# Kernel tuning notes

Hardware: AMD Instinct MI355X
Metric: run time of the kernel (lower is better)

The kernel has to match this reference:

```python
import jax, jax.numpy as jnp
import numpy as np
import math

PATCHES = [(2, 2), (4, 4), (8, 8), (16, 16)]  # (width, height) per scale
D_MODEL = 256
EPS = 1e-5


def setup_inputs() -> dict:
    key = jax.random.key(0)
    ks = jax.random.split(key, 12)
    b, c, h, w = 4, D_MODEL, 128, 128
    s = 1.0 / math.sqrt(c)
    inp = {
        'x': jax.random.normal(ks[0], (b, c, h, w), jnp.float32),
        'y': jax.random.normal(ks[1], (b, c, h, w), jnp.float32),
        'Wq': jax.random.normal(ks[2], (c, c), jnp.float32) * s,
        'bq': jnp.zeros((c,), jnp.float32),
        'Wk': jax.random.normal(ks[3], (c, c), jnp.float32) * s,
        'bk': jnp.zeros((c,), jnp.float32),
        'Wv': jax.random.normal(ks[4], (c, c), jnp.float32) * s,
        'bv': jnp.zeros((c,), jnp.float32),
        'Wo': jax.random.normal(ks[5], (c, c, 3, 3), jnp.float32) * (1.0 / math.sqrt(c * 9)),
        'bo': jnp.zeros((c,), jnp.float32),
        'gamma': jnp.ones((c,), jnp.float32),
        'beta': jnp.zeros((c,), jnp.float32),
    }
    return inp


def _conv1x1(x, W, b):
    # 1x1 conv == channel matmul
    return jnp.einsum('oc,bchw->bohw', W, x) + b[None, :, None, None]


def _windowed_attention(q, k, v, ww, hh):
    # q,k,v: [b, d_k, h, w] -> windows of (hh, ww), tokens = out_h*out_w
    b, d_k, h, w = q.shape
    out_h, out_w = h // hh, w // ww

    def to_tokens(t):
        t = t.reshape(b, d_k, out_h, hh, out_w, ww)
        t = t.transpose(0, 2, 4, 1, 3, 5)  # b, out_h, out_w, d_k, hh, ww
        return t.reshape(b, out_h * out_w, d_k * hh * ww)

    qt, kt, vt = to_tokens(q), to_tokens(k), to_tokens(v)
    scale = 1.0 / math.sqrt(qt.shape[-1])
    scores = jnp.einsum('bnd,bmd->bnm', qt, kt) * scale
    p = jax.nn.softmax(scores, axis=-1)
    out = jnp.einsum('bnm,bmd->bnd', p, vt)
    out = out.reshape(b, out_h, out_w, d_k, hh, ww)
    out = out.transpose(0, 3, 1, 4, 2, 5).reshape(b, d_k, h, w)
    return out


def reference(x, y, Wq, bq, Wk, bk, Wv, bv, Wo, bo, gamma, beta):
    b, c, h, w = x.shape
    n_scales = len(PATCHES)
    d_k = c // n_scales

    q_all = _conv1x1(x, Wq, bq)
    k_all = _conv1x1(y, Wk, bk)
    v_all = _conv1x1(y, Wv, bv)

    outs = []
    for i, (ww, hh) in enumerate(PATCHES):
        sl = slice(i * d_k, (i + 1) * d_k)
        outs.append(_windowed_attention(q_all[:, sl], k_all[:, sl], v_all[:, sl], ww, hh))
    out = jnp.concatenate(outs, axis=1)  # [b, c, h, w]

    # output_linear: Conv3x3 (pad 1) -> BatchNorm2d (batch stats) -> LeakyReLU(0.2)
    z = jax.lax.conv_general_dilated(
        out, Wo, window_strides=(1, 1), padding='SAME',
        dimension_numbers=('NCHW', 'OIHW', 'NCHW')) + bo[None, :, None, None]
    mean = jnp.mean(z, axis=(0, 2, 3), keepdims=True)
    var = jnp.var(z, axis=(0, 2, 3), keepdims=True)
    zn = (z - mean) * jax.lax.rsqrt(var + EPS)
    zn = zn * gamma[None, :, None, None] + beta[None, :, None, None]
    return jnp.where(zn >= 0, zn, 0.2 * zn)
```

## Files before the change

### kernel.cpp

```cpp
#include <hip/hip_runtime.h>
#include <math.h>

#define BN 4
#define CC 256
#define HH_ 128
#define WW_ 128
#define HWP (HH_*WW_)
#define TOK (64*HWP)


typedef __attribute__((ext_vector_type(8))) short bf16x8;
typedef __attribute__((ext_vector_type(4))) float f32x4;

__device__ __forceinline__ float bf2f(unsigned short u) {
    return __uint_as_float(((unsigned)u) << 16);
}
__device__ __forceinline__ unsigned short f2bf(float f) {
    unsigned u = __float_as_uint(f);
    u += 0x7FFF + ((u >> 16) & 1);
    return (unsigned short)(u >> 16);
}
__device__ __forceinline__ void load4f(const unsigned short* p, float o[4]) {
    ushort4 v = *(const ushort4*)p;
    o[0] = bf2f(v.x); o[1] = bf2f(v.y); o[2] = bf2f(v.z); o[3] = bf2f(v.w);
}
__device__ __forceinline__ float ld1(const unsigned short* p) { return bf2f(*p); }
__device__ __forceinline__ float ld1(const float* p) { return *p; }
__device__ __forceinline__ void st1(unsigned short* p, float v) { *p = f2bf(v); }
__device__ __forceinline__ void st1(float* p, float v) { *p = v; }

#define LDS_STRIDE 72

struct Tile32 { uint4 v[4]; };

__device__ __forceinline__ Tile32 load_tile_bf16(
    const unsigned short* src, size_t stride, int t)
{
    int r = t >> 1, kc = (t & 1) * 32;
    const uint4* sp = (const uint4*)(src + (size_t)r * stride + kc);
    Tile32 o;
    o.v[0] = sp[0]; o.v[1] = sp[1]; o.v[2] = sp[2]; o.v[3] = sp[3];
    return o;
}

__device__ __forceinline__ Tile32 load_tile_f32(
    const float* src, size_t stride, int t)
{
    int r = t >> 1, kc = (t & 1) * 32;
    const float4* sp = (const float4*)(src + (size_t)r * stride + kc);
    unsigned short tmp[32];
    #pragma unroll
    for (int i = 0; i < 8; i++) {
        float4 v = sp[i];
        tmp[i*4+0] = f2bf(v.x); tmp[i*4+1] = f2bf(v.y);
        tmp[i*4+2] = f2bf(v.z); tmp[i*4+3] = f2bf(v.w);
    }
    Tile32 o;
    const uint4* tp = (const uint4*)tmp;
    o.v[0] = tp[0]; o.v[1] = tp[1]; o.v[2] = tp[2]; o.v[3] = tp[3];
    return o;
}

__device__ __forceinline__ void store_tile(
    unsigned short* lds, const Tile32& d, int t)
{
    int r = t >> 1, kc = (t & 1) * 32;
    uint4* dp = (uint4*)&lds[r * LDS_STRIDE + kc];
    dp[0] = d.v[0]; dp[1] = d.v[1]; dp[2] = d.v[2]; dp[3] = d.v[3];
}

__device__ __forceinline__ void mfma_iter(
    const unsigned short* As, const unsigned short* Bs,
    int wm, int wn, int lr, int quad, f32x4 acc[4][4])
{
    #pragma unroll
    for (int s = 0; s < 2; s++) {
        bf16x8 af[4], bfr[4];
        #pragma unroll
        for (int i = 0; i < 4; i++)
            af[i] = *(const bf16x8*)&As[(wm*64 + i*16 + lr) * LDS_STRIDE + s*32 + quad*8];
        #pragma unroll
        for (int j = 0; j < 4; j++)
            bfr[j] = *(const bf16x8*)&Bs[(wn*64 + j*16 + lr) * LDS_STRIDE + s*32 + quad*8];
        #pragma unroll
        for (int i = 0; i < 4; i++)
            #pragma unroll
            for (int j = 0; j < 4; j++)
                acc[i][j] = __builtin_amdgcn_mfma_f32_16x16x32_bf16(
                    af[i], bfr[j], acc[i][j], 0, 0, 0);
    }
}

__global__ __launch_bounds__(256) void zero_kernel(float* __restrict__ p)
{
    p[blockIdx.x * 256 + threadIdx.x] = 0.f;
}

__global__ __launch_bounds__(256) void nchw_to_nhwc(
    const float* __restrict__ x, const float* __restrict__ y,
    unsigned short* __restrict__ xt, unsigned short* __restrict__ yt)
{
    __shared__ unsigned short T[64 * 72];
    int z = blockIdx.z;
    int b = z & 3, which = z >> 2;
    const float* src = (which ? y : x) + (size_t)b * CC * HWP;
    unsigned short* dst = (which ? yt : xt) + (size_t)b * HWP * CC;
    int p0 = blockIdx.x * 64, c0 = blockIdx.y * 64;
    int t = threadIdx.x;

    int cl = t >> 2, pc = (t & 3) * 16;
    #pragma unroll
    for (int e = 0; e < 16; e += 4) {
        float4 v = *(const float4*)&src[(size_t)(c0 + cl) * HWP + p0 + pc + e];
        T[(pc + e + 0) * 72 + cl] = f2bf(v.x);
        T[(pc + e + 1) * 72 + cl] = f2bf(v.y);
        T[(pc + e + 2) * 72 + cl] = f2bf(v.z);
        T[(pc + e + 3) * 72 + cl] = f2bf(v.w);
    }
    __syncthreads();
    int p = t >> 2, cc = (t & 3) * 16;
    uint4 a = *(uint4*)&T[p * 72 + cc];
    uint4 bsec = *(uint4*)&T[p * 72 + cc + 8];
    uint4* dp = (uint4*)&dst[(size_t)(p0 + p) * CC + c0 + cc];
    dp[0] = a; dp[1] = bsec;
}

__global__ __launch_bounds__(256) void wpack_kernel(
    const float* __restrict__ Wo, unsigned short* __restrict__ wpack)
{
    int o = blockIdx.x, c = threadIdx.x;
    const float* wr = Wo + ((size_t)o * CC + c) * 9;
    #pragma unroll
    for (int tap = 0; tap < 9; tap++)
        wpack[((size_t)o * 9 + tap) * CC + c] = f2bf(wr[tap]);
}

__global__ __launch_bounds__(256) void proj_gemm(
    const unsigned short* __restrict__ xt, const unsigned short* __restrict__ yt,
    const float* __restrict__ Wq, const float* __restrict__ bq,
    const float* __restrict__ Wk, const float* __restrict__ bk,
    const float* __restrict__ Wv, const float* __restrict__ bv,
    unsigned short* __restrict__ qt, unsigned short* __restrict__ kt,
    unsigned short* __restrict__ vt)
{
    __shared__ unsigned short As[128 * LDS_STRIDE], Bs[128 * LDS_STRIDE];
    int z = blockIdx.z, b = z & 3, which = z >> 2;
    const unsigned short* src = (which == 0) ? xt : yt;
    const float* Wm   = (which == 0) ? Wq : (which == 1 ? Wk : Wv);
    const float* bias = (which == 0) ? bq : (which == 1 ? bk : bv);
    unsigned short* outp = (which == 0) ? qt : (which == 1 ? kt : vt);

    int m0 = blockIdx.y * 128;
    int n0 = blockIdx.x * 128;
    const float* A = Wm + (size_t)m0 * CC;
    const unsigned short* B = src + ((size_t)b * HWP + n0) * CC;

    int t = threadIdx.x, w = t >> 6, lane = t & 63;
    int quad = lane >> 4, lr = lane & 15, wm = w >> 1, wn = w & 1;

    f32x4 acc[4][4];
    #pragma unroll
    for (int i = 0; i < 4; i++)
        #pragma unroll
        for (int j = 0; j < 4; j++) acc[i][j] = (f32x4){0.f, 0.f, 0.f, 0.f};

    for (int k0 = 0; k0 < CC; k0 += 64) {
        Tile32 ta = load_tile_f32(A + k0, CC, t);
        Tile32 tb = load_tile_bf16(B + k0, CC, t);
        __syncthreads();
        store_tile(As, ta, t); store_tile(Bs, tb, t);
        __syncthreads();
        mfma_iter(As, Bs, wm, wn, lr, quad, acc);
    }

    #pragma unroll
    for (int i = 0; i < 4; i++) {
        int obase = m0 + wm * 64 + i * 16 + quad * 4;
        #pragma unroll
        for (int rr = 0; rr < 4; rr++) {
            int o = obase + rr;
            int s = o >> 6, lg = s + 1;
            int ch = o & 63;
            float bia = bias[o];
            unsigned short* ob = outp + ((size_t)s * 4 + b) * TOK;
            #pragma unroll
            for (int j = 0; j < 4; j++) {
                int p = n0 + wn * 64 + j * 16 + lr;
                int yy = p >> 7, xx = p & 127;
                int oy = yy >> lg, wy = yy & ((1 << lg) - 1);
                int ox = xx >> lg, wx = xx & ((1 << lg) - 1);
                int tokn = (oy << (7 - lg)) + ox;
                int didx = (ch << (2 * lg)) + (wy << lg) + wx;
                size_t idx;
                if (which == 2 && s < 3)
                    idx = ((size_t)didx << (14 - 2 * lg)) + tokn;
                else
                    idx = ((size_t)tokn << (6 + 2 * lg)) + didx;
                ob[idx] = f2bf(acc[i][j][rr] + bia);
            }
        }
    }
}

template<int NTOK, int DD>
__global__ __launch_bounds__(256) void s_gemm_exp(
    const unsigned short* __restrict__ Qb, const unsigned short* __restrict__ Kb,
    unsigned short* __restrict__ S0, unsigned short* __restrict__ S1,
    float* __restrict__ rsg, float sc)
{
    __shared__ unsigned short As[128 * LDS_STRIDE], Bs[128 * LDS_STRIDE];
    int bz = blockIdx.z;
    int m0 = blockIdx.y * 128, n0 = blockIdx.x * 128;
    const unsigned short* Q = Qb + (size_t)bz * TOK + (size_t)m0 * DD;
    const unsigned short* K = Kb + (size_t)bz * TOK + (size_t)n0 * DD;
    unsigned short* S;
    if (S1) S = bz ? S1 : S0;
    else    S = S0 + (size_t)bz * NTOK * NTOK;
    float* rs = rsg + (size_t)bz * NTOK;

    int t = threadIdx.x, w = t >> 6, lane = t & 63;
    int quad = lane >> 4, lr = lane & 15, wm = w >> 1, wn = w & 1;

    f32x4 acc[4][4];
    #pragma unroll
    for (int i = 0; i < 4; i++)
        #pragma unroll
        for (int j = 0; j < 4; j++) acc[i][j] = (f32x4){0.f, 0.f, 0.f, 0.f};

    for (int k0 = 0; k0 < DD; k0 += 64) {
        Tile32 ta = load_tile_bf16(Q + k0, DD, t);
        Tile32 tb = load_tile_bf16(K + k0, DD, t);
        __syncthreads();
        store_tile(As, ta, t); store_tile(Bs, tb, t);
        __syncthreads();
        mfma_iter(As, Bs, wm, wn, lr, quad, acc);
    }

    #pragma unroll
    for (int i = 0; i < 4; i++) {
        int m = m0 + wm * 64 + i * 16 + quad * 4;
        float rsum[4] = {0.f, 0.f, 0.f, 0.f};
        #pragma unroll
        for (int j = 0; j < 4; j++) {
            int n = n0 + wn * 64 + j * 16 + lr;
            #pragma unroll
            for (int rr = 0; rr < 4; rr++) {
                float e = __expf(acc[i][j][rr] * sc);
                S[(size_t)(m + rr) * NTOK + n] = f2bf(e);
                rsum[rr] += e;
            }
        }
        #pragma unroll
        for (int rr = 0; rr < 4; rr++) {
            float v = rsum[rr];
            v += __shfl_xor(v, 1);
            v += __shfl_xor(v, 2);
            v += __shfl_xor(v, 4);
            v += __shfl_xor(v, 8);
            if (lr == 0) atomicAdd(&rs[m + rr], v);
        }
    }
}

template<int NTOK, int DD, int LG, int CH0>
__global__ __launch_bounds__(256) void o_gemm(
    const unsigned short* __restrict__ Pb, const unsigned short* __restrict__ Vb,
    const float* __restrict__ rsg, unsigned short* __restrict__ aot, int b0)
{
    __shared__ unsigned short As[128 * LDS_STRIDE], Bs[128 * LDS_STRIDE];
    int bz = blockIdx.z, b = b0 + bz;
    int m0 = blockIdx.y * 128, n0 = blockIdx.x * 128;
    const unsigned short* P = Pb + (size_t)bz * NTOK * NTOK + (size_t)m0 * NTOK;
    const unsigned short* V = Vb + (size_t)bz * TOK + (size_t)n0 * NTOK;
    const float* rs = rsg + (size_t)bz * NTOK;

    int t = threadIdx.x, w = t >> 6, lane = t & 63;
    int quad = lane >> 4, lr = lane & 15, wm = w >> 1, wn = w & 1;

    f32x4 acc[4][4];
    #pragma unroll
    for (int i = 0; i < 4; i++)
        #pragma unroll
        for (int j = 0; j < 4; j++) acc[i][j] = (f32x4){0.f, 0.f, 0.f, 0.f};

    for (int k0 = 0; k0 < NTOK; k0 += 64) {
        Tile32 ta = load_tile_bf16(P + k0, NTOK, t);
        Tile32 tb = load_tile_bf16(V + k0, NTOK, t);
        __syncthreads();
        store_tile(As, ta, t); store_tile(Bs, tb, t);
        __syncthreads();
        mfma_iter(As, Bs, wm, wn, lr, quad, acc);
    }

    #pragma unroll
    for (int i = 0; i < 4; i++) {
        int tb0 = m0 + wm * 64 + i * 16 + quad * 4;
        #pragma unroll
        for (int rr = 0; rr < 4; rr++) {
            int tokn = tb0 + rr;
            float inv = 1.f / rs[tokn];
            int oy = tokn >> (7 - LG), ox = tokn & ((1 << (7 - LG)) - 1);
            #pragma unroll
            for (int j = 0; j < 4; j++) {
                int d = n0 + wn * 64 + j * 16 + lr;
                int ch = d >> (2 * LG);
                int r2 = d & ((1 << (2 * LG)) - 1);
                int wy = r2 >> LG, wx = r2 & ((1 << LG) - 1);
                int yy = (oy << LG) + wy, xx = (ox << LG) + wx;
                aot[((size_t)b * HWP + yy * WW_ + xx) * CC + CH0 + ch] =
                    f2bf(acc[i][j][rr] * inv);
            }
        }
    }
}

__global__ __launch_bounds__(256) void o0_split(
    const unsigned short* __restrict__ P0, const unsigned short* __restrict__ P1,
    const unsigned short* __restrict__ Vb, float* __restrict__ part)
{
    __shared__ unsigned short As[128 * LDS_STRIDE], Bs[128 * LDS_STRIDE];
    int bz = blockIdx.z;
    int bsel = bz >> 2, sp = bz & 3;
    int m0 = blockIdx.y * 128;
    int n0 = blockIdx.x * 128;
    const unsigned short* P = (bsel ? P1 : P0) + (size_t)m0 * 4096 + sp * 1024;
    const unsigned short* V = Vb + (size_t)bsel * TOK + (size_t)n0 * 4096 + sp * 1024;
    float* op = part + (size_t)bz * TOK;

    int t = threadIdx.x, w = t >> 6, lane = t & 63;
    int quad = lane >> 4, lr = lane & 15, wm = w >> 1, wn = w & 1;

    f32x4 acc[4][4];
    #pragma unroll
    for (int i = 0; i < 4; i++)
        #pragma unroll
        for (int j = 0; j < 4; j++) acc[i][j] = (f32x4){0.f, 0.f, 0.f, 0.f};

    for (int k0 = 0; k0 < 1024; k0 += 64) {
        Tile32 ta = load_tile_bf16(P + k0, 4096, t);
        Tile32 tb = load_tile_bf16(V + k0, 4096, t);
        __syncthreads();
        store_tile(As, ta, t); store_tile(Bs, tb, t);
        __syncthreads();
        mfma_iter(As, Bs, wm, wn, lr, quad, acc);
    }

    #pragma unroll
    for (int i = 0; i < 4; i++) {
        int tb0 = m0 + wm * 64 + i * 16 + quad * 4;
        #pragma unroll
        for (int rr = 0; rr < 4; rr++) {
            int tokn = tb0 + rr;
            #pragma unroll
            for (int j = 0; j < 4; j++) {
                int d = n0 + wn * 64 + j * 16 + lr;
                op[(size_t)tokn * 256 + d] = acc[i][j][rr];
            }
        }
    }
}

__global__ __launch_bounds__(256) void combine0(
    const float* __restrict__ part, const float* __restrict__ rs,
    unsigned short* __restrict__ aot, int b0)
{
    int bsel = blockIdx.y, b = b0 + bsel;
    int tok0 = blockIdx.x * 16;
    const float* p = part + (size_t)bsel * 4 * TOK;
    int t = threadIdx.x;
    int w = t >> 6, ch = t & 63;
    int wy = w >> 1, wx = w & 1;
    #pragma unroll 4
    for (int u = 0; u < 16; u++) {
        int tok = tok0 + u;
        size_t base = (size_t)tok * 256 + ch * 4 + w;
        float v = p[base] + p[base + TOK] + p[base + 2 * (size_t)TOK]
                + p[base + 3 * (size_t)TOK];
        v *= 1.f / rs[(size_t)bsel * 4096 + tok];
        int oy = tok >> 6, ox = tok & 63;
        int yy = oy * 2 + wy, xx = ox * 2 + wx;
        aot[((size_t)b * HWP + yy * WW_ + xx) * CC + ch] = f2bf(v);
    }
}

__device__ __forceinline__ Tile32 load_tile_conv(
    const unsigned short* aob, int ys, int dx, int cbase, int t)
{
    int r = t >> 1, kc = (t & 1) * 32;
    int xs = r + dx;
    Tile32 o;
    if (ys >= 0 && ys < HH_ && xs >= 0 && xs < WW_) {
        const uint4* sp = (const uint4*)(aob + ((size_t)ys * WW_ + xs) * CC + cbase + kc);
        o.v[0] = sp[0]; o.v[1] = sp[1]; o.v[2] = sp[2]; o.v[3] = sp[3];
    } else {
        uint4 zz = make_uint4(0, 0, 0, 0);
        o.v[0] = zz; o.v[1] = zz; o.v[2] = zz; o.v[3] = zz;
    }
    return o;
}

__global__ __launch_bounds__(256) void conv_gemm(
    const unsigned short* __restrict__ aot, const unsigned short* __restrict__ wpack,
    const float* __restrict__ bo, float* __restrict__ zout)
{
    __shared__ unsigned short As[128 * LDS_STRIDE], Bs[128 * LDS_STRIDE];
    int yrow = blockIdx.x;
    int o0 = blockIdx.y * 128;
    int b = blockIdx.z;
    const unsigned short* aob = aot + (size_t)b * HWP * CC;
    const unsigned short* wsrc = wpack + (size_t)o0 * 2304;

    int t = threadIdx.x, w = t >> 6, lane = t & 63;
    int quad = lane >> 4, lr = lane & 15, wm = w >> 1, wn = w & 1;

    f32x4 acc[4][4];
    #pragma unroll
    for (int i = 0; i < 4; i++)
        #pragma unroll
        for (int j = 0; j < 4; j++) acc[i][j] = (f32x4){0.f, 0.f, 0.f, 0.f};

    for (int tap = 0; tap < 9; tap++) {
        int dy = tap / 3 - 1, dx = tap % 3 - 1;
        int ys = yrow + dy;
        for (int cb = 0; cb < CC; cb += 64) {
            Tile32 ta = load_tile_bf16(wsrc + tap * CC + cb, 2304, t);
            Tile32 tb = load_tile_conv(aob, ys, dx, cb, t);
            __syncthreads();
            store_tile(As, ta, t); store_tile(Bs, tb, t);
            __syncthreads();
            mfma_iter(As, Bs, wm, wn, lr, quad, acc);
        }
    }

    #pragma unroll
    for (int i = 0; i < 4; i++) {
        int ob = o0 + wm * 64 + i * 16 + quad * 4;
        #pragma unroll
        for (int j = 0; j < 4; j++) {
            int x = wn * 64 + j * 16 + lr;
            #pragma unroll
            for (int rr = 0; rr < 4; rr++) {
                int o = ob + rr;
                zout[((size_t)(b * CC + o)) * HWP + yrow * WW_ + x] =
                    acc[i][j][rr] + bo[o];
            }
        }
    }
}

__global__ __launch_bounds__(256) void s3_kernel(
    const unsigned short* __restrict__ Qb, const unsigned short* __restrict__ Kb,
    float* __restrict__ S, float sc)
{
    const int N = 64, D = 16384, KLEN = 1024;
    int b = blockIdx.z >> 4, kc = blockIdx.z & 15;
    const unsigned short* Q = Qb + (size_t)b * TOK;
    const unsigned short* K = Kb + (size_t)b * TOK;
    float* Sb = S + (size_t)b * N * N;
    int k0 = kc * KLEN;

    __shared__ float As[16][64], Bs[16][64];
    int t = threadIdx.x, tx = t & 15, ty = t >> 4, r = t >> 2, q = t & 3;

    float acc[4][4] = {};
    for (int kk = k0; kk < k0 + KLEN; kk += 16) {
        float a4[4], b4[4];
        load4f(&Q[(size_t)r * D + kk + q * 4], a4);
        load4f(&K[(size_t)r * D + kk + q * 4], b4);
        __syncthreads();
        As[q*4+0][r] = a4[0]; As[q*4+1][r] = a4[1]; As[q*4+2][r] = a4[2]; As[q*4+3][r] = a4[3];
        Bs[q*4+0][r] = b4[0]; Bs[q*4+1][r] = b4[1]; Bs[q*4+2][r] = b4[2]; Bs[q*4+3][r] = b4[3];
        __syncthreads();
        #pragma unroll
        for (int k = 0; k < 16; k++) {
            float4 af = *(const float4*)&As[k][ty*4];
            float4 bf = *(const float4*)&Bs[k][tx*4];
            float ar[4] = {af.x, af.y, af.z, af.w};
            float br[4] = {bf.x, bf.y, bf.z, bf.w};
            #pragma unroll
            for (int ii = 0; ii < 4; ii++)
                #pragma unroll
                for (int jj = 0; jj < 4; jj++)
                    acc[ii][jj] = fmaf(ar[ii], br[jj], acc[ii][jj]);
        }
    }

    #pragma unroll
    for (int ii = 0; ii < 4; ii++)
        #pragma unroll
        for (int jj = 0; jj < 4; jj++)
            atomicAdd(&Sb[(size_t)(ty * 4 + ii) * N + tx * 4 + jj], acc[ii][jj] * sc);
}

template<typename T>
__global__ __launch_bounds__(256) void softmax_kernel(T* __restrict__ S, int n)
{
    int b = blockIdx.y;
    int row = blockIdx.x;
    T* rp = S + (size_t)b * n * n + (size_t)row * n;
    __shared__ float red[256];
    int t = threadIdx.x;

    float m = -1e30f;
    for (int j = t; j < n; j += 256) m = fmaxf(m, ld1(&rp[j]));
    red[t] = m; __syncthreads();
    for (int s = 128; s > 0; s >>= 1) { if (t < s) red[t] = fmaxf(red[t], red[t + s]); __syncthreads(); }
    m = red[0]; __syncthreads();

    float sum = 0.f;
    for (int j = t; j < n; j += 256) { float e = __expf(ld1(&rp[j]) - m); st1(&rp[j], e); sum += e; }
    red[t] = sum; __syncthreads();
    for (int s = 128; s > 0; s >>= 1) { if (t < s) red[t] += red[t + s]; __syncthreads(); }
    float inv = 1.f / red[0];
    for (int j = t; j < n; j += 256) st1(&rp[j], ld1(&rp[j]) * inv);
}

__global__ __launch_bounds__(256) void o3_kernel(
    const float* __restrict__ P, const unsigned short* __restrict__ Vb,
    unsigned short* __restrict__ aot)
{
    const int N = 64, D = 16384, LG = 4, CH0 = 192;
    int bz = blockIdx.z;
    const float* Pb = P + (size_t)bz * N * N;
    const unsigned short* V = Vb + (size_t)bz * TOK;
    int i0 = blockIdx.x * 64, d0 = blockIdx.y * 64;

    __shared__ float Ps[16][64];
    __shared__ float Vs[16][64];
    int t = threadIdx.x, tx = t & 15, ty = t >> 4, r = t >> 2, q = t & 3;
    int vr = t >> 4, vq = t & 15;

    float acc[4][4] = {};
    for (int j0 = 0; j0 < N; j0 += 16) {
        float p4[4], v4[4];
        float4 pv = *(const float4*)&Pb[(size_t)(i0 + r) * N + j0 + q * 4];
        p4[0] = pv.x; p4[1] = pv.y; p4[2] = pv.z; p4[3] = pv.w;
        load4f(&V[(size_t)(j0 + vr) * D + d0 + vq * 4], v4);
        __syncthreads();
        Ps[q*4+0][r] = p4[0]; Ps[q*4+1][r] = p4[1]; Ps[q*4+2][r] = p4[2]; Ps[q*4+3][r] = p4[3];
        Vs[vr][vq*4+0] = v4[0]; Vs[vr][vq*4+1] = v4[1]; Vs[vr][vq*4+2] = v4[2]; Vs[vr][vq*4+3] = v4[3];
        __syncthreads();
        #pragma unroll
        for (int k = 0; k < 16; k++) {
            float4 pf = *(const float4*)&Ps[k][ty*4];
            float4 vf = *(const float4*)&Vs[k][tx*4];
            float pr[4] = {pf.x, pf.y, pf.z, pf.w};
            float vrr[4] = {vf.x, vf.y, vf.z, vf.w};
            #pragma unroll
            for (int ii = 0; ii < 4; ii++)
                #pragma unroll
                for (int jj = 0; jj < 4; jj++)
                    acc[ii][jj] = fmaf(pr[ii], vrr[jj], acc[ii][jj]);
        }
    }

    #pragma unroll
    for (int ii = 0; ii < 4; ii++) {
        int tokn = i0 + ty * 4 + ii;
        int oy = tokn >> (7 - LG), ox = tokn & ((1 << (7 - LG)) - 1);
        #pragma unroll
        for (int jj = 0; jj < 4; jj++) {
            int d = d0 + tx * 4 + jj;
            int ch = d >> (2 * LG);
            int r2 = d & ((1 << (2 * LG)) - 1);
            int wy = r2 >> LG, wx = r2 & ((1 << LG) - 1);
            int yy = (oy << LG) + wy, xx = (ox << LG) + wx;
            aot[((size_t)bz * HWP + yy * WW_ + xx) * CC + CH0 + ch] = f2bf(acc[ii][jj]);
        }
    }
}

__global__ __launch_bounds__(256) void bn_stats_kernel(
    const float* __restrict__ z, const float* __restrict__ gamma,
    const float* __restrict__ beta, float* __restrict__ stats)
{
    int c = blockIdx.x;
    int t = threadIdx.x;
    float s = 0.f, s2 = 0.f;
    for (int i = t; i < BN * HWP; i += 256) {
        int b = i >> 14, p = i & (HWP - 1);
        float v = z[(((size_t)b * CC + c) << 14) + p];
        s += v; s2 = fmaf(v, v, s2);
    }
    __shared__ float r1[256], r2[256];
    r1[t] = s; r2[t] = s2; __syncthreads();
    for (int st = 128; st > 0; st >>= 1) {
        if (t < st) { r1[t] += r1[t + st]; r2[t] += r2[t + st]; }
        __syncthreads();
    }
    if (t == 0) {
        float inv_n = 1.f / (BN * HWP);
        float mean = r1[0] * inv_n;
        float var = r2[0] * inv_n - mean * mean;
        float rstd = rsqrtf(var + 1e-5f);
        float gs = gamma[c] * rstd;
        stats[c] = gs;
        stats[CC + c] = beta[c] - mean * gs;
    }
}

__global__ __launch_bounds__(256) void bn_apply_kernel(
    float* __restrict__ z, const float* __restrict__ stats)
{
    size_t i4 = (size_t)blockIdx.x * 256 + threadIdx.x;
    size_t idx = i4 * 4;
    int c = (int)((idx >> 14) & 255);
    float gs = stats[c], gb = stats[CC + c];
    float4 v = *(float4*)&z[idx];
    v.x = fmaf(v.x, gs, gb); v.y = fmaf(v.y, gs, gb);
    v.z = fmaf(v.z, gs, gb); v.w = fmaf(v.w, gs, gb);
    v.x = v.x >= 0.f ? v.x : 0.2f * v.x;
    v.y = v.y >= 0.f ? v.y : 0.2f * v.y;
    v.z = v.z >= 0.f ? v.z : 0.2f * v.z;
    v.w = v.w >= 0.f ? v.w : 0.2f * v.w;
    *(float4*)&z[idx] = v;
}

extern "C" void kernel_launch(void* const* d_in, const int* in_sizes, int n_in,
                              void* d_out, int out_size, void* d_ws, size_t ws_size,
                              hipStream_t stream)
{
    const float* x     = (const float*)d_in[0];
    const float* y     = (const float*)d_in[1];
    const float* Wq    = (const float*)d_in[2];
    const float* bq    = (const float*)d_in[3];
    const float* Wk    = (const float*)d_in[4];
    const float* bk    = (const float*)d_in[5];
    const float* Wv    = (const float*)d_in[6];
    const float* bv    = (const float*)d_in[7];
    const float* Wo    = (const float*)d_in[8];
    const float* bo    = (const float*)d_in[9];
    const float* gamma = (const float*)d_in[10];
    const float* beta  = (const float*)d_in[11];
    float* out = (float*)d_out;

    unsigned short* qt    = (unsigned short*)d_ws;
    unsigned short* kt    = qt + (size_t)16777216;
    unsigned short* vt    = kt + (size_t)16777216;
    unsigned short* aot   = vt + (size_t)16777216;
    unsigned short* Sbf   = aot + (size_t)16777216;
    unsigned short* wpack = Sbf + (size_t)16777216;
    float* stats = (float*)(wpack + (size_t)589824);
    float* S3    = stats + 512;
    float* rs0   = S3 + 16384;
    float* rs1   = rs0 + 16384;
    float* rs2   = rs1 + 4096;
    unsigned short* xt = Sbf;
    unsigned short* yt = aot;
    unsigned short* Sout = (unsigned short*)d_out;
    float* part = (float*)((char*)d_out + (size_t)33554432);

    dim3 blk(256);

    zero_kernel<<<dim3(148), blk, 0, stream>>>(S3);
    nchw_to_nhwc<<<dim3(256, 4, 8), blk, 0, stream>>>(x, y, xt, yt);
    wpack_kernel<<<dim3(256), blk, 0, stream>>>(Wo, wpack);

    proj_gemm<<<dim3(128, 2, 12), blk, 0, stream>>>(
        xt, yt, Wq, bq, Wk, bk, Wv, bv, qt, kt, vt);

    for (int pr = 0; pr < 2; pr++) {
        int b0 = pr * 2;
        s_gemm_exp<4096, 256><<<dim3(32, 32, 2), blk, 0, stream>>>(
            qt + (size_t)b0 * TOK, kt + (size_t)b0 * TOK,
            Sbf, Sout, rs0 + (size_t)b0 * 4096, 1.f / 16.f);
        o0_split<<<dim3(2, 32, 8), blk, 0, stream>>>(
            Sbf, Sout, vt + (size_t)b0 * TOK, part);
        combine0<<<dim3(256, 2), blk, 0, stream>>>(
            part, rs0 + (size_t)b0 * 4096, aot, b0);
    }
    s_gemm_exp<1024, 1024><<<dim3(8, 8, 4), blk, 0, stream>>>(
        qt + (size_t)4 * TOK, kt + (size_t)4 * TOK, Sbf, nullptr, rs1, 1.f / 32.f);
    o_gemm<1024, 1024, 2, 64><<<dim3(8, 8, 4), blk, 0, stream>>>(
        Sbf, vt + (size_t)4 * TOK, rs1, aot, 0);
    s_gemm_exp<256, 4096><<<dim3(2, 2, 4), blk, 0, stream>>>(
        qt + (size_t)8 * TOK, kt + (size_t)8 * TOK, Sbf, nullptr, rs2, 1.f / 64.f);
    o_gemm<256, 4096, 3, 128><<<dim3(32, 2, 4), blk, 0, stream>>>(
        Sbf, vt + (size_t)8 * TOK, rs2, aot, 0);
    s3_kernel<<<dim3(1, 1, 64), blk, 0, stream>>>(
        qt + (size_t)12 * TOK, kt + (size_t)12 * TOK, S3, 1.f / 128.f);
    softmax_kernel<float><<<dim3(64, 4), blk, 0, stream>>>(S3, 64);
    o3_kernel<<<dim3(1, 256, 4), blk, 0, stream>>>(S3, vt + (size_t)12 * TOK, aot);

    conv_gemm<<<dim3(128, 2, 4), blk, 0, stream>>>(aot, wpack, bo, out);
    bn_stats_kernel<<<dim3(CC), blk, 0, stream>>>(out, gamma, beta, stats);
    bn_apply_kernel<<<dim3(16384), blk, 0, stream>>>(out, stats);
}
```

Measured before the change: 902.9 us.

## Fuse scale-0 attention into flash kernel, split-K scale-2 scores, fuse BN stats

```diff
diff --git a/kernel.cpp b/kernel.cpp
--- a/kernel.cpp
+++ b/kernel.cpp
@@ -202,20 +202,170 @@
     }
 }
 
+#define PS_STRIDE 136
+
+__global__ __launch_bounds__(512) void flash0(
+    const unsigned short* __restrict__ qt, const unsigned short* __restrict__ kt,
+    const unsigned short* __restrict__ vt, unsigned short* __restrict__ aot)
+{
+    __shared__ unsigned short Ps[64 * PS_STRIDE];
+    __shared__ unsigned short Bs[256 * LDS_STRIDE];
+
+    int L = blockIdx.x;
+    int xcd = L & 7, slot = L >> 3;
+    int b = xcd >> 1;
+    int q0 = (slot + 32 * (xcd & 1)) * 64;
+
+    const unsigned short* Qb = qt + (size_t)b * TOK;
+    const unsigned short* Kb = kt + (size_t)b * TOK;
+    const unsigned short* Vb = vt + (size_t)b * TOK;
+
+    int t = threadIdx.x, w = t >> 6, lane = t & 63;
+    int quad = lane >> 4, lr = lane & 15;
+    int wm = w >> 2, wn = w & 3;
+
+    bf16x8 aq[4][2][2];
+    #pragma unroll
+    for (int k = 0; k < 4; k++)
+        #pragma unroll
+        for (int s = 0; s < 2; s++)
+            #pragma unroll
+            for (int i = 0; i < 2; i++)
+                aq[k][s][i] = *(const bf16x8*)&Qb[
+                    (size_t)(q0 + wm*32 + i*16 + lr) * 256 + k*64 + s*32 + quad*8];
+
+    f32x4 acc_o[2][4];
+    #pragma unroll
+    for (int i = 0; i < 2; i++)
+        #pragma unroll
+        for (int j = 0; j < 4; j++) acc_o[i][j] = (f32x4){0.f, 0.f, 0.f, 0.f};
+    float rsum[2][4] = {};
+
+    const float SC = 1.f / 16.f;
+    int sr = t >> 1, sc_ = (t & 1) * 32;
+
+    for (int kv0 = 0; kv0 < 4096; kv0 += 128) {
+        f32x4 acc_s[2][2];
+        #pragma unroll
+        for (int i = 0; i < 2; i++)
+            #pragma unroll
+            for (int j = 0; j < 2; j++) acc_s[i][j] = (f32x4){0.f, 0.f, 0.f, 0.f};
+
+        #pragma unroll
+        for (int kp = 0; kp < 2; kp++) {
+            __syncthreads();
+            {
+                const uint4* sp = (const uint4*)&Kb[
+                    (size_t)(kv0 + (sr & 127)) * 256 + kp*128 + (sr >> 7)*64 + sc_];
+                uint4* dp = (uint4*)&Bs[sr * LDS_STRIDE + sc_];
+                dp[0] = sp[0]; dp[1] = sp[1]; dp[2] = sp[2]; dp[3] = sp[3];
+            }
+            __syncthreads();
+            #pragma unroll
+            for (int t2 = 0; t2 < 2; t2++)
+                #pragma unroll
+                for (int s = 0; s < 2; s++) {
+                    bf16x8 bfr[2];
+                    #pragma unroll
+                    for (int j = 0; j < 2; j++)
+                        bfr[j] = *(const bf16x8*)&Bs[
+                            (t2*128 + wn*32 + j*16 + lr) * LDS_STRIDE + s*32 + quad*8];
+                    #pragma unroll
+                    for (int i = 0; i < 2; i++)
+                        #pragma unroll
+                        for (int j = 0; j < 2; j++)
+                            acc_s[i][j] = __builtin_amdgcn_mfma_f32_16x16x32_bf16(
+                                aq[kp*2 + t2][s][i], bfr[j], acc_s[i][j], 0, 0, 0);
+                }
+        }
+
+        #pragma unroll
+        for (int i = 0; i < 2; i++)
+            #pragma unroll
+            for (int j = 0; j < 2; j++)
+                #pragma unroll
+                for (int rr = 0; rr < 4; rr++) {
+                    float e = __expf(acc_s[i][j][rr] * SC);
+                    Ps[(wm*32 + i*16 + quad*4 + rr) * PS_STRIDE + wn*32 + j*16 + lr]
+                        = f2bf(e);
+                    rsum[i][rr] += e;
+                }
+
+        #pragma unroll
+        for (int ks = 0; ks < 2; ks++) {
+            __syncthreads();
+            {
+                const uint4* sp = (const uint4*)&Vb[
+                    (size_t)sr * 4096 + kv0 + ks*64 + sc_];
+                uint4* dp = (uint4*)&Bs[sr * LDS_STRIDE + sc_];
+                dp[0] = sp[0]; dp[1] = sp[1]; dp[2] = sp[2]; dp[3] = sp[3];
+            }
+            __syncthreads();
+            #pragma unroll
+            for (int s = 0; s < 2; s++) {
+                bf16x8 pa[2], vb[4];
+                #pragma unroll
+                for (int i = 0; i < 2; i++)
+                    pa[i] = *(const bf16x8*)&Ps[
+                        (wm*32 + i*16 + lr) * PS_STRIDE + ks*64 + s*32 + quad*8];
+                #pragma unroll
+                for (int j = 0; j < 4; j++)
+                    vb[j] = *(const bf16x8*)&Bs[
+                        (wn*64 + j*16 + lr) * LDS_STRIDE + s*32 + quad*8];
+                #pragma unroll
+                for (int i = 0; i < 2; i++)
+                    #pragma unroll
+                    for (int j = 0; j < 4; j++)
+                        acc_o[i][j] = __builtin_amdgcn_mfma_f32_16x16x32_bf16(
+                            pa[i], vb[j], acc_o[i][j], 0, 0, 0);
+            }
+        }
+    }
+
+    __syncthreads();
+    float* rsred = (float*)Ps;
+    #pragma unroll
+    for (int i = 0; i < 2; i++)
+        #pragma unroll
+        for (int rr = 0; rr < 4; rr++) {
+            float v = rsum[i][rr];
+            v += __shfl_xor(v, 1); v += __shfl_xor(v, 2);
+            v += __shfl_xor(v, 4); v += __shfl_xor(v, 8);
+            if (lr == 0)
+                rsred[wn*64 + wm*32 + i*16 + quad*4 + rr] = v;
+        }
+    __syncthreads();
+    #pragma unroll
+    for (int i = 0; i < 2; i++)
+        #pragma unroll
+        for (int rr = 0; rr < 4; rr++) {
+            int tl = wm*32 + i*16 + quad*4 + rr;
+            float inv = 1.f / (rsred[tl] + rsred[64 + tl]
+                             + rsred[128 + tl] + rsred[192 + tl]);
+            int tokn = q0 + tl;
+            int oy = tokn >> 6, ox = tokn & 63;
+            #pragma unroll
+            for (int j = 0; j < 4; j++) {
+                int d = wn*64 + j*16 + lr;
+                int ch = d >> 2, wp = d & 3;
+                int yy = oy*2 + (wp >> 1), xx = ox*2 + (wp & 1);
+                aot[((size_t)b * HWP + yy * WW_ + xx) * CC + ch]
+                    = f2bf(acc_o[i][j][rr] * inv);
+            }
+        }
+}
+
 template<int NTOK, int DD>
 __global__ __launch_bounds__(256) void s_gemm_exp(
     const unsigned short* __restrict__ Qb, const unsigned short* __restrict__ Kb,
-    unsigned short* __restrict__ S0, unsigned short* __restrict__ S1,
-    float* __restrict__ rsg, float sc)
+    unsigned short* __restrict__ S0, float* __restrict__ rsg, float sc)
 {
     __shared__ unsigned short As[128 * LDS_STRIDE], Bs[128 * LDS_STRIDE];
     int bz = blockIdx.z;
     int m0 = blockIdx.y * 128, n0 = blockIdx.x * 128;
     const unsigned short* Q = Qb + (size_t)bz * TOK + (size_t)m0 * DD;
     const unsigned short* K = Kb + (size_t)bz * TOK + (size_t)n0 * DD;
-    unsigned short* S;
-    if (S1) S = bz ? S1 : S0;
-    else    S = S0 + (size_t)bz * NTOK * NTOK;
+    unsigned short* S = S0 + (size_t)bz * NTOK * NTOK;
     float* rs = rsg + (size_t)bz * NTOK;
 
     int t = threadIdx.x, w = t >> 6, lane = t & 63;
@@ -314,18 +464,16 @@
     }
 }
 
-__global__ __launch_bounds__(256) void o0_split(
-    const unsigned short* __restrict__ P0, const unsigned short* __restrict__ P1,
-    const unsigned short* __restrict__ Vb, float* __restrict__ part)
+__global__ __launch_bounds__(256) void s2_partial(
+    const unsigned short* __restrict__ Qb, const unsigned short* __restrict__ Kb,
+    float* __restrict__ S2p)
 {
     __shared__ unsigned short As[128 * LDS_STRIDE], Bs[128 * LDS_STRIDE];
-    int bz = blockIdx.z;
-    int bsel = bz >> 2, sp = bz & 3;
-    int m0 = blockIdx.y * 128;
-    int n0 = blockIdx.x * 128;
-    const unsigned short* P = (bsel ? P1 : P0) + (size_t)m0 * 4096 + sp * 1024;
-    const unsigned short* V = Vb + (size_t)bsel * TOK + (size_t)n0 * 4096 + sp * 1024;
-    float* op = part + (size_t)bz * TOK;
+    int z = blockIdx.z, b = z >> 3, sp = z & 7;
+    int m0 = blockIdx.y * 128, n0 = blockIdx.x * 128;
+    const unsigned short* Q = Qb + (size_t)b * TOK + (size_t)m0 * 4096;
+    const unsigned short* K = Kb + (size_t)b * TOK + (size_t)n0 * 4096;
+    float* So = S2p + ((size_t)(sp * 4 + b)) * 65536;
 
     int t = threadIdx.x, w = t >> 6, lane = t & 63;
     int quad = lane >> 4, lr = lane & 15, wm = w >> 1, wn = w & 1;
@@ -336,9 +484,10 @@
         #pragma unroll
         for (int j = 0; j < 4; j++) acc[i][j] = (f32x4){0.f, 0.f, 0.f, 0.f};
 
-    for (int k0 = 0; k0 < 1024; k0 += 64) {
-        Tile32 ta = load_tile_bf16(P + k0, 4096, t);
-        Tile32 tb = load_tile_bf16(V + k0, 4096, t);
+    int kend = sp * 512 + 512;
+    for (int k0 = sp * 512; k0 < kend; k0 += 64) {
+        Tile32 ta = load_tile_bf16(Q + k0, 4096, t);
+        Tile32 tb = load_tile_bf16(K + k0, 4096, t);
         __syncthreads();
         store_tile(As, ta, t); store_tile(Bs, tb, t);
         __syncthreads();
@@ -347,40 +496,35 @@
 
     #pragma unroll
     for (int i = 0; i < 4; i++) {
-        int tb0 = m0 + wm * 64 + i * 16 + quad * 4;
-        #pragma unroll
-        for (int rr = 0; rr < 4; rr++) {
-            int tokn = tb0 + rr;
-            #pragma unroll
-            for (int j = 0; j < 4; j++) {
-                int d = n0 + wn * 64 + j * 16 + lr;
-                op[(size_t)tokn * 256 + d] = acc[i][j][rr];
-            }
-        }
-    }
-}
-
-__global__ __launch_bounds__(256) void combine0(
-    const float* __restrict__ part, const float* __restrict__ rs,
-    unsigned short* __restrict__ aot, int b0)
-{
-    int bsel = blockIdx.y, b = b0 + bsel;
-    int tok0 = blockIdx.x * 16;
-    const float* p = part + (size_t)bsel * 4 * TOK;
-    int t = threadIdx.x;
-    int w = t >> 6, ch = t & 63;
-    int wy = w >> 1, wx = w & 1;
-    #pragma unroll 4
-    for (int u = 0; u < 16; u++) {
-        int tok = tok0 + u;
-        size_t base = (size_t)tok * 256 + ch * 4 + w;
-        float v = p[base] + p[base + TOK] + p[base + 2 * (size_t)TOK]
-                + p[base + 3 * (size_t)TOK];
-        v *= 1.f / rs[(size_t)bsel * 4096 + tok];
-        int oy = tok >> 6, ox = tok & 63;
-        int yy = oy * 2 + wy, xx = ox * 2 + wx;
-        aot[((size_t)b * HWP + yy * WW_ + xx) * CC + ch] = f2bf(v);
-    }
+        int m = m0 + wm * 64 + i * 16 + quad * 4;
+        #pragma unroll
+        for (int j = 0; j < 4; j++) {
+            int n = n0 + wn * 64 + j * 16 + lr;
+            #pragma unroll
+            for (int rr = 0; rr < 4; rr++)
+                So[(size_t)(m + rr) * 256 + n] = acc[i][j][rr];
+        }
+    }
+}
+
+__global__ __launch_bounds__(256) void s2_finish(
+    const float* __restrict__ S2p, unsigned short* __restrict__ Sbf,
+    float* __restrict__ rs2, float sc)
+{
+    int row = blockIdx.x, b = blockIdx.y, t = threadIdx.x;
+    float v = 0.f;
+    #pragma unroll
+    for (int sp = 0; sp < 8; sp++)
+        v += S2p[((size_t)(sp * 4 + b)) * 65536 + row * 256 + t];
+    float e = __expf(v * sc);
+    Sbf[((size_t)b * 65536) + row * 256 + t] = f2bf(e);
+    __shared__ float red[256];
+    red[t] = e; __syncthreads();
+    for (int s = 128; s > 0; s >>= 1) {
+        if (t < s) red[t] += red[t + s];
+        __syncthreads();
+    }
+    if (t == 0) rs2[b * 256 + row] = red[0];
 }
 
 __device__ __forceinline__ Tile32 load_tile_conv(
@@ -401,7 +545,8 @@
 
 __global__ __launch_bounds__(256) void conv_gemm(
     const unsigned short* __restrict__ aot, const unsigned short* __restrict__ wpack,
-    const float* __restrict__ bo, float* __restrict__ zout)
+    const float* __restrict__ bo, float* __restrict__ zout,
+    float* __restrict__ stats)
 {
     __shared__ unsigned short As[128 * LDS_STRIDE], Bs[128 * LDS_STRIDE];
     int yrow = blockIdx.x;
@@ -434,18 +579,42 @@
 
     #pragma unroll
     for (int i = 0; i < 4; i++) {
-        int ob = o0 + wm * 64 + i * 16 + quad * 4;
-        #pragma unroll
-        for (int j = 0; j < 4; j++) {
-            int x = wn * 64 + j * 16 + lr;
-            #pragma unroll
-            for (int rr = 0; rr < 4; rr++) {
-                int o = ob + rr;
-                zout[((size_t)(b * CC + o)) * HWP + yrow * WW_ + x] =
-                    acc[i][j][rr] + bo[o];
+        #pragma unroll
+        for (int rr = 0; rr < 4; rr++) {
+            int o = o0 + wm * 64 + i * 16 + quad * 4 + rr;
+            float bia = bo[o];
+            float s1 = 0.f, s2v = 0.f;
+            #pragma unroll
+            for (int j = 0; j < 4; j++) {
+                int x = wn * 64 + j * 16 + lr;
+                float v = acc[i][j][rr] + bia;
+                zout[((size_t)(b * CC + o)) * HWP + yrow * WW_ + x] = v;
+                s1 += v; s2v = fmaf(v, v, s2v);
             }
-        }
-    }
+            s1 += __shfl_xor(s1, 1); s2v += __shfl_xor(s2v, 1);
+            s1 += __shfl_xor(s1, 2); s2v += __shfl_xor(s2v, 2);
+            s1 += __shfl_xor(s1, 4); s2v += __shfl_xor(s2v, 4);
+            s1 += __shfl_xor(s1, 8); s2v += __shfl_xor(s2v, 8);
+            if (lr == 0) {
+                atomicAdd(&stats[o], s1);
+                atomicAdd(&stats[CC + o], s2v);
+            }
+        }
+    }
+}
+
+__global__ __launch_bounds__(256) void stats_finalize(
+    float* __restrict__ stats, const float* __restrict__ gamma,
+    const float* __restrict__ beta)
+{
+    int c = threadIdx.x;
+    const float inv_n = 1.f / (BN * HWP);
+    float mean = stats[c] * inv_n;
+    float var = stats[CC + c] * inv_n - mean * mean;
+    float rstd = rsqrtf(var + 1e-5f);
+    float gs = gamma[c] * rstd;
+    stats[c] = gs;
+    stats[CC + c] = beta[c] - mean * gs;
 }
 
 __global__ __launch_bounds__(256) void s3_kernel(
@@ -567,35 +736,6 @@
             int yy = (oy << LG) + wy, xx = (ox << LG) + wx;
             aot[((size_t)bz * HWP + yy * WW_ + xx) * CC + CH0 + ch] = f2bf(acc[ii][jj]);
         }
-    }
-}
-
-__global__ __launch_bounds__(256) void bn_stats_kernel(
-    const float* __restrict__ z, const float* __restrict__ gamma,
-    const float* __restrict__ beta, float* __restrict__ stats)
-{
-    int c = blockIdx.x;
-    int t = threadIdx.x;
-    float s = 0.f, s2 = 0.f;
-    for (int i = t; i < BN * HWP; i += 256) {
-        int b = i >> 14, p = i & (HWP - 1);
-        float v = z[(((size_t)b * CC + c) << 14) + p];
-        s += v; s2 = fmaf(v, v, s2);
-    }
-    __shared__ float r1[256], r2[256];
-    r1[t] = s; r2[t] = s2; __syncthreads();
-    for (int st = 128; st > 0; st >>= 1) {
-        if (t < st) { r1[t] += r1[t + st]; r2[t] += r2[t + st]; }
-        __syncthreads();
-    }
-    if (t == 0) {
-        float inv_n = 1.f / (BN * HWP);
-        float mean = r1[0] * inv_n;
-        float var = r2[0] * inv_n - mean * mean;
-        float rstd = rsqrtf(var + 1e-5f);
-        float gs = gamma[c] * rstd;
-        stats[c] = gs;
-        stats[CC + c] = beta[c] - mean * gs;
     }
 }
 
@@ -645,44 +785,39 @@
     float* rs0   = S3 + 16384;
     float* rs1   = rs0 + 16384;
     float* rs2   = rs1 + 4096;
+    (void)rs0;
     unsigned short* xt = Sbf;
     unsigned short* yt = aot;
-    unsigned short* Sout = (unsigned short*)d_out;
-    float* part = (float*)((char*)d_out + (size_t)33554432);
+    float* S2p = (float*)d_out;
 
     dim3 blk(256);
 
-    zero_kernel<<<dim3(148), blk, 0, stream>>>(S3);
+    zero_kernel<<<dim3(150), blk, 0, stream>>>(stats);
     nchw_to_nhwc<<<dim3(256, 4, 8), blk, 0, stream>>>(x, y, xt, yt);
     wpack_kernel<<<dim3(256), blk, 0, stream>>>(Wo, wpack);
 
     proj_gemm<<<dim3(128, 2, 12), blk, 0, stream>>>(
         xt, yt, Wq, bq, Wk, bk, Wv, bv, qt, kt, vt);
 
-    for (int pr = 0; pr < 2; pr++) {
-        int b0 = pr * 2;
-        s_gemm_exp<4096, 256><<<dim3(32, 32, 2), blk, 0, stream>>>(
-            qt + (size_t)b0 * TOK, kt + (size_t)b0 * TOK,
-            Sbf, Sout, rs0 + (size_t)b0 * 4096, 1.f / 16.f);
-        o0_split<<<dim3(2, 32, 8), blk, 0, stream>>>(
-            Sbf, Sout, vt + (size_t)b0 * TOK, part);
-        combine0<<<dim3(256, 2), blk, 0, stream>>>(
-            part, rs0 + (size_t)b0 * 4096, aot, b0);
-    }
+    flash0<<<dim3(256), dim3(512), 0, stream>>>(qt, kt, vt, aot);
+
     s_gemm_exp<1024, 1024><<<dim3(8, 8, 4), blk, 0, stream>>>(
-        qt + (size_t)4 * TOK, kt + (size_t)4 * TOK, Sbf, nullptr, rs1, 1.f / 32.f);
+        qt + (size_t)4 * TOK, kt + (size_t)4 * TOK, Sbf, rs1, 1.f / 32.f);
     o_gemm<1024, 1024, 2, 64><<<dim3(8, 8, 4), blk, 0, stream>>>(
         Sbf, vt + (size_t)4 * TOK, rs1, aot, 0);
-    s_gemm_exp<256, 4096><<<dim3(2, 2, 4), blk, 0, stream>>>(
-        qt + (size_t)8 * TOK, kt + (size_t)8 * TOK, Sbf, nullptr, rs2, 1.f / 64.f);
+
+    s2_partial<<<dim3(2, 2, 32), blk, 0, stream>>>(
+        qt + (size_t)8 * TOK, kt + (size_t)8 * TOK, S2p);
+    s2_finish<<<dim3(256, 4), blk, 0, stream>>>(S2p, Sbf, rs2, 1.f / 64.f);
     o_gemm<256, 4096, 3, 128><<<dim3(32, 2, 4), blk, 0, stream>>>(
         Sbf, vt + (size_t)8 * TOK, rs2, aot, 0);
+
     s3_kernel<<<dim3(1, 1, 64), blk, 0, stream>>>(
         qt + (size_t)12 * TOK, kt + (size_t)12 * TOK, S3, 1.f / 128.f);
     softmax_kernel<float><<<dim3(64, 4), blk, 0, stream>>>(S3, 64);
     o3_kernel<<<dim3(1, 256, 4), blk, 0, stream>>>(S3, vt + (size_t)12 * TOK, aot);
 
-    conv_gemm<<<dim3(128, 2, 4), blk, 0, stream>>>(aot, wpack, bo, out);
-    bn_stats_kernel<<<dim3(CC), blk, 0, stream>>>(out, gamma, beta, stats);
+    conv_gemm<<<dim3(128, 2, 4), blk, 0, stream>>>(aot, wpack, bo, out, stats);
+    stats_finalize<<<dim3(1), blk, 0, stream>>>(stats, gamma, beta);
     bn_apply_kernel<<<dim3(16384), blk, 0, stream>>>(out, stats);
 }
```

After: 880.2 us. 2.5% less time.
